# Kernel tuning notes

Measured on AMD Instinct MI355X. Metric: run time of the kernel, lower is better.

## Reference

```python
import jax, jax.numpy as jnp
import numpy as np

N = 50000        # nodes
E = 100000       # directed edges
F_NODE = 22      # atom features
F_EDGE = 4       # bond features
H = 64           # hidden_dim
EPS = 1e-5       # BatchNorm eps


def setup_inputs() -> dict:
    key = jax.random.key(0)
    ks = jax.random.split(key, 16)
    s = 0.05
    return {
        "x": jax.random.normal(ks[0], (N, F_NODE), dtype=jnp.float32),
        "edge_attr": jax.random.normal(ks[1], (E, F_EDGE), dtype=jnp.float32),
        "We1": jax.random.normal(ks[2], (F_EDGE, F_NODE * H), dtype=jnp.float32) * s,
        "be1": jnp.zeros((F_NODE * H,), dtype=jnp.float32),
        "root1": jax.random.normal(ks[3], (F_NODE, H), dtype=jnp.float32) * s,
        "b1": jnp.zeros((H,), dtype=jnp.float32),
        "g1": jnp.ones((H,), dtype=jnp.float32),
        "beta1": jnp.zeros((H,), dtype=jnp.float32),
        "We2": jax.random.normal(ks[4], (F_EDGE, H * H), dtype=jnp.float32) * s,
        "be2": jnp.zeros((H * H,), dtype=jnp.float32),
        "root2": jax.random.normal(ks[5], (H, H), dtype=jnp.float32) * s,
        "b2": jnp.zeros((H,), dtype=jnp.float32),
        "g2": jnp.ones((H,), dtype=jnp.float32),
        "beta2": jnp.zeros((H,), dtype=jnp.float32),
        "Wfc": jax.random.normal(ks[6], (H, 1), dtype=jnp.float32) * s,
        "bfc": jnp.zeros((1,), dtype=jnp.float32),
        "edge_index": jax.random.randint(ks[7], (2, E), 0, N, dtype=jnp.int32),
    }


def nnconv(x, edge_index, edge_attr, We, be, root, bias, in_ch, out_ch):
    # PyG NNConv (aggr='add', root_weight=True):
    #   out_i = x_i @ root + bias + sum_{(j->i)} x_j @ reshape(MLP(e_ji), [in, out])
    src, dst = edge_index[0], edge_index[1]
    w = jax.nn.relu(edge_attr @ We + be).reshape(-1, in_ch, out_ch)  # [E, in, out]
    msg = jnp.einsum('ei,eio->eo', x[src], w)                        # [E, out]
    agg = jax.ops.segment_sum(msg, dst, num_segments=x.shape[0])     # [N, out]
    return agg + x @ root + bias


def batchnorm(x, gamma, beta):
    # training-mode BatchNorm1d: batch statistics, biased variance
    mu = jnp.mean(x, axis=0)
    var = jnp.mean(jnp.square(x - mu), axis=0)
    return (x - mu) * jax.lax.rsqrt(var + EPS) * gamma + beta


def reference(x, edge_attr, We1, be1, root1, b1, g1, beta1,
              We2, be2, root2, b2, g2, beta2, Wfc, bfc, edge_index):
    h = nnconv(x, edge_index, edge_attr, We1, be1, root1, b1, F_NODE, H)
    h = jax.nn.relu(batchnorm(h, g1, beta1))
    # dropout is identity in eval / deterministic reference
    h = nnconv(h, edge_index, edge_attr, We2, be2, root2, b2, H, H)
    h = jax.nn.relu(batchnorm(h, g2, beta2))
    return jax.nn.sigmoid(h @ Wfc + bfc)  # [N, 1]
```

## Files before the change

### kernel.cpp

```cpp
#include <hip/hip_runtime.h>
#include <math.h>

#define N_NODES 50000
#define N_EDGES 100000
#define FNODE 22
#define HDIM 64
#define BN_EPS 1e-5f

typedef __attribute__((ext_vector_type(8))) short bfrag;
typedef __attribute__((ext_vector_type(4))) float facc;
typedef __attribute__((ext_vector_type(4))) unsigned int uint4v;

__device__ __forceinline__ float readlane_f(float v, int lane) {
    return __uint_as_float(__builtin_amdgcn_readlane(__float_as_uint(v), (unsigned)lane));
}
__device__ __forceinline__ unsigned f2bf(float x) {
    unsigned u = __float_as_uint(x);
    return (u + 0x7FFFu + ((u >> 16) & 1u)) >> 16;
}
__device__ __forceinline__ unsigned pk2bf(float lo, float hi) {
    return f2bf(lo) | (f2bf(hi) << 16);
}

__global__ void k_node1(const float* __restrict__ x, const float* __restrict__ root1,
                        const float* __restrict__ b1, float* __restrict__ h1) {
    __shared__ float rt[FNODE * HDIM];
    for (int idx = threadIdx.x; idx < FNODE * HDIM; idx += blockDim.x) rt[idx] = root1[idx];
    __syncthreads();
    int lane = threadIdx.x & 63;
    int wpb = blockDim.x >> 6;
    int wid = blockIdx.x * wpb + (threadIdx.x >> 6);
    int nw = gridDim.x * wpb;
    const int ngroups = N_NODES / 8;
    float bload = b1[lane];
    for (int g = wid; g < ngroups; g += nw) {
        int nbase = g * 8;
        float xr[8], acc[8];
#pragma unroll
        for (int e = 0; e < 8; ++e) {
            xr[e] = (lane < FNODE) ? x[(nbase + e) * FNODE + lane] : 0.f;
            acc[e] = bload;
        }
#pragma unroll
        for (int i = 0; i < FNODE; ++i) {
            float r = rt[i * HDIM + lane];
#pragma unroll
            for (int e = 0; e < 8; ++e)
                acc[e] = fmaf(readlane_f(xr[e], i), r, acc[e]);
        }
#pragma unroll
        for (int e = 0; e < 8; ++e) h1[(nbase + e) * HDIM + lane] = acc[e];
    }
}

template <int IN, int CHUNK>
__launch_bounds__(256, 4)
__global__ void k_edge(const float* __restrict__ h, const float* __restrict__ ea,
                       const float* __restrict__ We, const float* __restrict__ be,
                       const int* __restrict__ eidx, float* __restrict__ out) {
    constexpr int INH = IN * HDIM;
    __shared__ uint4v Wf[IN * 32];

    int obeg = (blockIdx.x & 1) * 32;
    int tileblk = blockIdx.x >> 1;

    for (int idx = threadIdx.x; idx < IN * 32; idx += 256) {
        int i = idx >> 5, oloc = idx & 31;
        int c = i * HDIM + obeg + oloc;
        Wf[idx] = uint4v{pk2bf(We[c], We[INH + c]),
                         pk2bf(We[2 * INH + c], We[3 * INH + c]),
                         f2bf(be[c]), 0u};
    }
    __syncthreads();

    int lane = threadIdx.x & 63;
    int e16 = lane & 15;
    int orow4 = (lane >> 4) * 4;
    int tile = tileblk * 4 + (threadIdx.x >> 6);
    int ebase = tile * 32;
    if (ebase >= N_EDGES) return;

    bool act = lane < 16;
    float4 ea0 = ((const float4*)ea)[ebase + e16];
    float4 ea1 = ((const float4*)ea)[ebase + 16 + e16];
    unsigned aone = act ? 0x3F80u : 0u;
    bfrag A0 = __builtin_bit_cast(bfrag, uint4v{act ? pk2bf(ea0.x, ea0.y) : 0u,
                                                act ? pk2bf(ea0.z, ea0.w) : 0u, aone, 0u});
    bfrag A1 = __builtin_bit_cast(bfrag, uint4v{act ? pk2bf(ea1.x, ea1.y) : 0u,
                                                act ? pk2bf(ea1.z, ea1.w) : 0u, aone, 0u});

    const float* pA[4];
    const float* pB[4];
    int dA[4], dB[4];
#pragma unroll
    for (int j = 0; j < 4; ++j) {
        pA[j] = h + (size_t)eidx[ebase + orow4 + j] * IN;
        pB[j] = h + (size_t)eidx[ebase + 16 + orow4 + j] * IN;
        dA[j] = eidx[N_EDGES + ebase + orow4 + j];
        dB[j] = eidx[N_EDGES + ebase + 16 + orow4 + j];
    }

    const facc zero4 = {0.f, 0.f, 0.f, 0.f};
    facc m0[2] = {zero4, zero4}, m1[2] = {zero4, zero4};

    for (int i0 = 0; i0 < IN; i0 += CHUNK) {
        float hA[4][CHUNK], hB[4][CHUNK];
        if constexpr (CHUNK == 4) {
#pragma unroll
            for (int j = 0; j < 4; ++j) {
                float4 v = *(const float4*)(pA[j] + i0);
                hA[j][0] = v.x; hA[j][1] = v.y; hA[j][2] = v.z; hA[j][3] = v.w;
                float4 u = *(const float4*)(pB[j] + i0);
                hB[j][0] = u.x; hB[j][1] = u.y; hB[j][2] = u.z; hB[j][3] = u.w;
            }
        } else {
#pragma unroll
            for (int j = 0; j < 4; ++j) {
                float2 v = *(const float2*)(pA[j] + i0);
                hA[j][0] = v.x; hA[j][1] = v.y;
                float2 u = *(const float2*)(pB[j] + i0);
                hB[j][0] = u.x; hB[j][1] = u.y;
            }
        }
#pragma unroll
        for (int t = 0; t < 2; ++t) {
#pragma unroll
            for (int di = 0; di < CHUNK; ++di) {
                bfrag B = __builtin_bit_cast(bfrag, Wf[(i0 + di) * 32 + t * 16 + e16]);
                facc t0 = __builtin_amdgcn_mfma_f32_16x16x32_bf16(A0, B, zero4, 0, 0, 0);
                facc t1 = __builtin_amdgcn_mfma_f32_16x16x32_bf16(A1, B, zero4, 0, 0, 0);
#pragma unroll
                for (int j = 0; j < 4; ++j) {
                    m0[t][j] = fmaf(hA[j][di], fmaxf(t0[j], 0.f), m0[t][j]);
                    m1[t][j] = fmaf(hB[j][di], fmaxf(t1[j], 0.f), m1[t][j]);
                }
            }
        }
    }

#pragma unroll
    for (int t = 0; t < 2; ++t) {
#pragma unroll
        for (int j = 0; j < 4; ++j) {
            atomicAdd(&out[(size_t)dA[j] * HDIM + obeg + t * 16 + e16], m0[t][j]);
            atomicAdd(&out[(size_t)dB[j] * HDIM + obeg + t * 16 + e16], m1[t][j]);
        }
    }
}

__global__ void k_packB(const float* __restrict__ root2, uint4v* __restrict__ Bt) {
    int t = threadIdx.x;
    int ot = t >> 6, lane = t & 63;
    int o = ot * 16 + (lane & 15);
    int kg = lane >> 4;
#pragma unroll
    for (int q = 0; q < 2; ++q) {
        int ib = q * 32 + kg * 8;
        Bt[(ot * 2 + q) * 64 + lane] =
            uint4v{pk2bf(root2[(ib + 0) * HDIM + o], root2[(ib + 1) * HDIM + o]),
                   pk2bf(root2[(ib + 2) * HDIM + o], root2[(ib + 3) * HDIM + o]),
                   pk2bf(root2[(ib + 4) * HDIM + o], root2[(ib + 5) * HDIM + o]),
                   pk2bf(root2[(ib + 6) * HDIM + o], root2[(ib + 7) * HDIM + o])};
    }
}

__global__ void k_stats(const float* __restrict__ hbuf, float* stats) {
    int c = threadIdx.x & 63;
    int r = threadIdx.x >> 6;
    int rowsPer = blockDim.x >> 6;
    float s = 0.f, q = 0.f;
    for (int n = blockIdx.x * rowsPer + r; n < N_NODES; n += gridDim.x * rowsPer) {
        float v = hbuf[n * HDIM + c];
        s += v;
        q = fmaf(v, v, q);
    }
    __shared__ float ls[4][64], lq[4][64];
    ls[r][c] = s;
    lq[r][c] = q;
    __syncthreads();
    if (r == 0) {
        s = ls[0][c] + ls[1][c] + ls[2][c] + ls[3][c];
        q = lq[0][c] + lq[1][c] + lq[2][c] + lq[3][c];
        atomicAdd(&stats[c], s);
        atomicAdd(&stats[64 + c], q);
    }
}

__global__ void k_finalize(const float* stats_in, const float* __restrict__ g,
                           const float* __restrict__ beta, float* as_out) {
    int c = threadIdx.x;
    float mu = stats_in[c] * (1.f / N_NODES);
    float var = stats_in[64 + c] * (1.f / N_NODES) - mu * mu;
    var = fmaxf(var, 0.f);
    float a = g[c] * rsqrtf(var + BN_EPS);
    as_out[c] = a;
    as_out[64 + c] = beta[c] - mu * a;
}

__global__ void k_apply1(const float* h1, const float* __restrict__ as1,
                         const uint4v* __restrict__ Bt, const float* __restrict__ b2,
                         float* __restrict__ h1n, float* h2) {
    int lane = threadIdx.x & 63;
    int m = lane & 15, kg = lane >> 4, orow4 = (lane >> 4) * 4;
    int tile = blockIdx.x * 4 + (threadIdx.x >> 6);
    int nb = tile * 16;
    if (nb >= N_NODES) return;
    int node = nb + m;
    const float* hr = h1 + (size_t)node * HDIM;

    float4 a0 = *(const float4*)(as1 + kg * 8), a1 = *(const float4*)(as1 + kg * 8 + 4);
    float4 s0 = *(const float4*)(as1 + 64 + kg * 8), s1 = *(const float4*)(as1 + 64 + kg * 8 + 4);
    float4 a2 = *(const float4*)(as1 + 32 + kg * 8), a3 = *(const float4*)(as1 + 32 + kg * 8 + 4);
    float4 s2 = *(const float4*)(as1 + 96 + kg * 8), s3 = *(const float4*)(as1 + 96 + kg * 8 + 4);

    float4 v0 = *(const float4*)(hr + kg * 8), v1 = *(const float4*)(hr + kg * 8 + 4);
    float4 v2 = *(const float4*)(hr + 32 + kg * 8), v3 = *(const float4*)(hr + 32 + kg * 8 + 4);

    float r0[8], r1[8];
#pragma unroll
    for (int p = 0; p < 4; ++p) {
        r0[p]     = fmaxf(fmaf((&v0.x)[p], (&a0.x)[p], (&s0.x)[p]), 0.f);
        r0[p + 4] = fmaxf(fmaf((&v1.x)[p], (&a1.x)[p], (&s1.x)[p]), 0.f);
        r1[p]     = fmaxf(fmaf((&v2.x)[p], (&a2.x)[p], (&s2.x)[p]), 0.f);
        r1[p + 4] = fmaxf(fmaf((&v3.x)[p], (&a3.x)[p], (&s3.x)[p]), 0.f);
    }
    *(float4*)(h1n + (size_t)node * HDIM + kg * 8)     = float4{r0[0], r0[1], r0[2], r0[3]};
    *(float4*)(h1n + (size_t)node * HDIM + kg * 8 + 4) = float4{r0[4], r0[5], r0[6], r0[7]};
    *(float4*)(h1n + (size_t)node * HDIM + 32 + kg * 8)     = float4{r1[0], r1[1], r1[2], r1[3]};
    *(float4*)(h1n + (size_t)node * HDIM + 32 + kg * 8 + 4) = float4{r1[4], r1[5], r1[6], r1[7]};

    bfrag A0 = __builtin_bit_cast(bfrag, uint4v{pk2bf(r0[0], r0[1]), pk2bf(r0[2], r0[3]),
                                                pk2bf(r0[4], r0[5]), pk2bf(r0[6], r0[7])});
    bfrag A1 = __builtin_bit_cast(bfrag, uint4v{pk2bf(r1[0], r1[1]), pk2bf(r1[2], r1[3]),
                                                pk2bf(r1[4], r1[5]), pk2bf(r1[6], r1[7])});

    const facc zero4 = {0.f, 0.f, 0.f, 0.f};
#pragma unroll
    for (int ot = 0; ot < 4; ++ot) {
        bfrag B0 = __builtin_bit_cast(bfrag, Bt[(ot * 2 + 0) * 64 + lane]);
        bfrag B1 = __builtin_bit_cast(bfrag, Bt[(ot * 2 + 1) * 64 + lane]);
        facc d = __builtin_amdgcn_mfma_f32_16x16x32_bf16(A0, B0, zero4, 0, 0, 0);
        d = __builtin_amdgcn_mfma_f32_16x16x32_bf16(A1, B1, d, 0, 0, 0);
        float bv = b2[ot * 16 + m];
#pragma unroll
        for (int j = 0; j < 4; ++j)
            h2[(size_t)(nb + orow4 + j) * HDIM + ot * 16 + m] = d[j] + bv;
    }
}

__global__ void k_final(const float* __restrict__ h2, const float* __restrict__ as2,
                        const float* __restrict__ Wfc, const float* __restrict__ bfc,
                        float* __restrict__ out) {
    int lane = threadIdx.x & 63;
    int n = blockIdx.x * (blockDim.x >> 6) + (threadIdx.x >> 6);
    if (n >= N_NODES) return;
    float a = as2[lane], s = as2[64 + lane];
    float v = fmaxf(fmaf(h2[n * HDIM + lane], a, s), 0.f) * Wfc[lane];
#pragma unroll
    for (int off = 32; off > 0; off >>= 1) v += __shfl_xor(v, off, 64);
    if (lane == 0) out[n] = 1.f / (1.f + expf(-(v + bfc[0])));
}

extern "C" void kernel_launch(void* const* d_in, const int* in_sizes, int n_in,
                              void* d_out, int out_size, void* d_ws, size_t ws_size,
                              hipStream_t stream) {
    const float* x     = (const float*)d_in[0];
    const float* ea    = (const float*)d_in[1];
    const float* We1   = (const float*)d_in[2];
    const float* be1   = (const float*)d_in[3];
    const float* root1 = (const float*)d_in[4];
    const float* b1    = (const float*)d_in[5];
    const float* g1    = (const float*)d_in[6];
    const float* beta1 = (const float*)d_in[7];
    const float* We2   = (const float*)d_in[8];
    const float* be2   = (const float*)d_in[9];
    const float* root2 = (const float*)d_in[10];
    const float* b2    = (const float*)d_in[11];
    const float* g2    = (const float*)d_in[12];
    const float* beta2 = (const float*)d_in[13];
    const float* Wfc   = (const float*)d_in[14];
    const float* bfc   = (const float*)d_in[15];
    const int*   eidx  = (const int*)d_in[16];
    float* out = (float*)d_out;

    char* ws = (char*)d_ws;
    const size_t nbuf = (size_t)N_NODES * HDIM * sizeof(float);
    float* h1    = (float*)ws;
    float* h1n   = (float*)(ws + nbuf);
    float* h2    = h1;
    float* stats = (float*)(ws + 2 * nbuf);
    uint4v* Bt   = (uint4v*)(ws + 2 * nbuf + 4096);

    hipMemsetAsync(stats, 0, 512 * sizeof(float), stream);
    k_packB<<<1, 256, 0, stream>>>(root2, Bt);

    const int edgeBlocks = 2 * ((N_EDGES / 32 + 3) / 4);
    const int nodeBlocks = (N_NODES + 3) / 4;
    const int tileBlocks = (N_NODES / 16 + 3) / 4;

    k_node1<<<512, 256, 0, stream>>>(x, root1, b1, h1);
    k_edge<FNODE, 2><<<edgeBlocks, 256, 0, stream>>>(x, ea, We1, be1, eidx, h1);
    k_stats<<<256, 256, 0, stream>>>(h1, stats);
    k_finalize<<<1, 64, 0, stream>>>(stats, g1, beta1, stats + 128);
    k_apply1<<<tileBlocks, 256, 0, stream>>>(h1, stats + 128, Bt, b2, h1n, h2);
    k_edge<HDIM, 4><<<edgeBlocks, 256, 0, stream>>>(h1n, ea, We2, be2, eidx, h2);
    k_stats<<<256, 256, 0, stream>>>(h2, stats + 256);
    k_finalize<<<1, 64, 0, stream>>>(stats + 256, g2, beta2, stats + 384);
    k_final<<<nodeBlocks, 256, 0, stream>>>(h2, stats + 384, Wfc, bfc, out);
}
```

Measured before the change: 184.8 us.

## Use MFMA for layer-1 root transform and software-prefetch gathered rows in edge kernel

Replaces the scalar readlane-based x@root1 kernel with a bf16 MFMA kernel over 16-node tiles, using a generalized k_packB template to pre-pack root1. In the edge kernel, gathered source-row chunks are double-buffered so the next chunk's loads are issued before the current chunk's MFMA/FMA work. Byte offsets are kept as 32-bit values, and destination indices are loaded only just before the atomics to lower register pressure. The cost is extra prefetch registers and bf16 rounding of x in layer 1, which was fp32 before.

```diff
diff --git a/kernel.cpp b/kernel.cpp
--- a/kernel.cpp
+++ b/kernel.cpp
@@ -11,9 +11,6 @@
 typedef __attribute__((ext_vector_type(4))) float facc;
 typedef __attribute__((ext_vector_type(4))) unsigned int uint4v;
 
-__device__ __forceinline__ float readlane_f(float v, int lane) {
-    return __uint_as_float(__builtin_amdgcn_readlane(__float_as_uint(v), (unsigned)lane));
-}
 __device__ __forceinline__ unsigned f2bf(float x) {
     unsigned u = __float_as_uint(x);
     return (u + 0x7FFFu + ((u >> 16) & 1u)) >> 16;
@@ -22,34 +19,53 @@
     return f2bf(lo) | (f2bf(hi) << 16);
 }
 
-__global__ void k_node1(const float* __restrict__ x, const float* __restrict__ root1,
+template <int K>
+__global__ void k_packB(const float* __restrict__ W, uint4v* __restrict__ Bt) {
+    constexpr int NQ = (K + 31) / 32;
+    int t = threadIdx.x;
+    int ot = t >> 6, lane = t & 63;
+    int o = ot * 16 + (lane & 15);
+    int kg = lane >> 4;
+#pragma unroll
+    for (int q = 0; q < NQ; ++q) {
+        unsigned w[4];
+#pragma unroll
+        for (int p = 0; p < 4; ++p) {
+            int k0 = q * 32 + kg * 8 + 2 * p;
+            float lo = (k0 < K) ? W[k0 * HDIM + o] : 0.f;
+            float hi = (k0 + 1 < K) ? W[(k0 + 1) * HDIM + o] : 0.f;
+            w[p] = pk2bf(lo, hi);
+        }
+        Bt[(ot * NQ + q) * 64 + lane] = uint4v{w[0], w[1], w[2], w[3]};
+    }
+}
+
+__global__ void k_node1(const float* __restrict__ x, const uint4v* __restrict__ Bt1,
                         const float* __restrict__ b1, float* __restrict__ h1) {
-    __shared__ float rt[FNODE * HDIM];
-    for (int idx = threadIdx.x; idx < FNODE * HDIM; idx += blockDim.x) rt[idx] = root1[idx];
-    __syncthreads();
     int lane = threadIdx.x & 63;
-    int wpb = blockDim.x >> 6;
-    int wid = blockIdx.x * wpb + (threadIdx.x >> 6);
-    int nw = gridDim.x * wpb;
-    const int ngroups = N_NODES / 8;
-    float bload = b1[lane];
-    for (int g = wid; g < ngroups; g += nw) {
-        int nbase = g * 8;
-        float xr[8], acc[8];
-#pragma unroll
-        for (int e = 0; e < 8; ++e) {
-            xr[e] = (lane < FNODE) ? x[(nbase + e) * FNODE + lane] : 0.f;
-            acc[e] = bload;
-        }
-#pragma unroll
-        for (int i = 0; i < FNODE; ++i) {
-            float r = rt[i * HDIM + lane];
-#pragma unroll
-            for (int e = 0; e < 8; ++e)
-                acc[e] = fmaf(readlane_f(xr[e], i), r, acc[e]);
-        }
-#pragma unroll
-        for (int e = 0; e < 8; ++e) h1[(nbase + e) * HDIM + lane] = acc[e];
+    int m = lane & 15, kg = lane >> 4, orow4 = kg * 4;
+    int tile = blockIdx.x * 4 + (threadIdx.x >> 6);
+    int nb = tile * 16;
+    if (nb >= N_NODES) return;
+    const float* xr = x + (size_t)(nb + m) * FNODE;
+    float xv[8];
+#pragma unroll
+    for (int p = 0; p < 4; ++p) {
+        int c = kg * 8 + 2 * p;
+        float2 v = (c + 1 < FNODE) ? *(const float2*)(xr + c) : float2{0.f, 0.f};
+        xv[2 * p] = v.x; xv[2 * p + 1] = v.y;
+    }
+    bfrag A = __builtin_bit_cast(bfrag, uint4v{pk2bf(xv[0], xv[1]), pk2bf(xv[2], xv[3]),
+                                               pk2bf(xv[4], xv[5]), pk2bf(xv[6], xv[7])});
+    const facc zero4 = {0.f, 0.f, 0.f, 0.f};
+#pragma unroll
+    for (int ot = 0; ot < 4; ++ot) {
+        bfrag B = __builtin_bit_cast(bfrag, Bt1[ot * 64 + lane]);
+        facc d = __builtin_amdgcn_mfma_f32_16x16x32_bf16(A, B, zero4, 0, 0, 0);
+        float bv = b1[ot * 16 + m];
+#pragma unroll
+        for (int j = 0; j < 4; ++j)
+            h1[(size_t)(nb + orow4 + j) * HDIM + ot * 16 + m] = d[j] + bv;
     }
 }
 
@@ -89,37 +105,49 @@
     bfrag A1 = __builtin_bit_cast(bfrag, uint4v{act ? pk2bf(ea1.x, ea1.y) : 0u,
                                                 act ? pk2bf(ea1.z, ea1.w) : 0u, aone, 0u});
 
-    const float* pA[4];
-    const float* pB[4];
-    int dA[4], dB[4];
+    const char* hb = (const char*)h;
+    unsigned offA[4], offB[4];
 #pragma unroll
     for (int j = 0; j < 4; ++j) {
-        pA[j] = h + (size_t)eidx[ebase + orow4 + j] * IN;
-        pB[j] = h + (size_t)eidx[ebase + 16 + orow4 + j] * IN;
-        dA[j] = eidx[N_EDGES + ebase + orow4 + j];
-        dB[j] = eidx[N_EDGES + ebase + 16 + orow4 + j];
+        offA[j] = (unsigned)eidx[ebase + orow4 + j] * (IN * 4);
+        offB[j] = (unsigned)eidx[ebase + 16 + orow4 + j] * (IN * 4);
     }
 
     const facc zero4 = {0.f, 0.f, 0.f, 0.f};
     facc m0[2] = {zero4, zero4}, m1[2] = {zero4, zero4};
 
+    float cA[4][CHUNK], cB[4][CHUNK];
+#pragma unroll
+    for (int j = 0; j < 4; ++j) {
+        if constexpr (CHUNK == 4) {
+            float4 v = *(const float4*)(hb + offA[j]);
+            cA[j][0] = v.x; cA[j][1] = v.y; cA[j][2] = v.z; cA[j][3] = v.w;
+            float4 u = *(const float4*)(hb + offB[j]);
+            cB[j][0] = u.x; cB[j][1] = u.y; cB[j][2] = u.z; cB[j][3] = u.w;
+        } else {
+            float2 v = *(const float2*)(hb + offA[j]);
+            cA[j][0] = v.x; cA[j][1] = v.y;
+            float2 u = *(const float2*)(hb + offB[j]);
+            cB[j][0] = u.x; cB[j][1] = u.y;
+        }
+    }
+
+#pragma unroll
     for (int i0 = 0; i0 < IN; i0 += CHUNK) {
-        float hA[4][CHUNK], hB[4][CHUNK];
-        if constexpr (CHUNK == 4) {
-#pragma unroll
-            for (int j = 0; j < 4; ++j) {
-                float4 v = *(const float4*)(pA[j] + i0);
-                hA[j][0] = v.x; hA[j][1] = v.y; hA[j][2] = v.z; hA[j][3] = v.w;
-                float4 u = *(const float4*)(pB[j] + i0);
-                hB[j][0] = u.x; hB[j][1] = u.y; hB[j][2] = u.z; hB[j][3] = u.w;
-            }
-        } else {
-#pragma unroll
-            for (int j = 0; j < 4; ++j) {
-                float2 v = *(const float2*)(pA[j] + i0);
-                hA[j][0] = v.x; hA[j][1] = v.y;
-                float2 u = *(const float2*)(pB[j] + i0);
-                hB[j][0] = u.x; hB[j][1] = u.y;
+        const int ip = (i0 + CHUNK < IN) ? (i0 + CHUNK) : i0;
+        float nA[4][CHUNK], nB[4][CHUNK];
+#pragma unroll
+        for (int j = 0; j < 4; ++j) {
+            if constexpr (CHUNK == 4) {
+                float4 v = *(const float4*)(hb + offA[j] + (size_t)ip * 4);
+                nA[j][0] = v.x; nA[j][1] = v.y; nA[j][2] = v.z; nA[j][3] = v.w;
+                float4 u = *(const float4*)(hb + offB[j] + (size_t)ip * 4);
+                nB[j][0] = u.x; nB[j][1] = u.y; nB[j][2] = u.z; nB[j][3] = u.w;
+            } else {
+                float2 v = *(const float2*)(hb + offA[j] + (size_t)ip * 4);
+                nA[j][0] = v.x; nA[j][1] = v.y;
+                float2 u = *(const float2*)(hb + offB[j] + (size_t)ip * 4);
+                nB[j][0] = u.x; nB[j][1] = u.y;
             }
         }
 #pragma unroll
@@ -131,13 +159,23 @@
                 facc t1 = __builtin_amdgcn_mfma_f32_16x16x32_bf16(A1, B, zero4, 0, 0, 0);
 #pragma unroll
                 for (int j = 0; j < 4; ++j) {
-                    m0[t][j] = fmaf(hA[j][di], fmaxf(t0[j], 0.f), m0[t][j]);
-                    m1[t][j] = fmaf(hB[j][di], fmaxf(t1[j], 0.f), m1[t][j]);
+                    m0[t][j] = fmaf(cA[j][di], fmaxf(t0[j], 0.f), m0[t][j]);
+                    m1[t][j] = fmaf(cB[j][di], fmaxf(t1[j], 0.f), m1[t][j]);
                 }
             }
         }
-    }
-
+#pragma unroll
+        for (int j = 0; j < 4; ++j)
+#pragma unroll
+            for (int di = 0; di < CHUNK; ++di) { cA[j][di] = nA[j][di]; cB[j][di] = nB[j][di]; }
+    }
+
+    int dA[4], dB[4];
+#pragma unroll
+    for (int j = 0; j < 4; ++j) {
+        dA[j] = eidx[N_EDGES + ebase + orow4 + j];
+        dB[j] = eidx[N_EDGES + ebase + 16 + orow4 + j];
+    }
 #pragma unroll
     for (int t = 0; t < 2; ++t) {
 #pragma unroll
@@ -145,22 +183,6 @@
             atomicAdd(&out[(size_t)dA[j] * HDIM + obeg + t * 16 + e16], m0[t][j]);
             atomicAdd(&out[(size_t)dB[j] * HDIM + obeg + t * 16 + e16], m1[t][j]);
         }
-    }
-}
-
-__global__ void k_packB(const float* __restrict__ root2, uint4v* __restrict__ Bt) {
-    int t = threadIdx.x;
-    int ot = t >> 6, lane = t & 63;
-    int o = ot * 16 + (lane & 15);
-    int kg = lane >> 4;
-#pragma unroll
-    for (int q = 0; q < 2; ++q) {
-        int ib = q * 32 + kg * 8;
-        Bt[(ot * 2 + q) * 64 + lane] =
-            uint4v{pk2bf(root2[(ib + 0) * HDIM + o], root2[(ib + 1) * HDIM + o]),
-                   pk2bf(root2[(ib + 2) * HDIM + o], root2[(ib + 3) * HDIM + o]),
-                   pk2bf(root2[(ib + 4) * HDIM + o], root2[(ib + 5) * HDIM + o]),
-                   pk2bf(root2[(ib + 6) * HDIM + o], root2[(ib + 7) * HDIM + o])};
     }
 }
 
@@ -289,20 +311,22 @@
     float* h1n   = (float*)(ws + nbuf);
     float* h2    = h1;
     float* stats = (float*)(ws + 2 * nbuf);
-    uint4v* Bt   = (uint4v*)(ws + 2 * nbuf + 4096);
+    uint4v* Bt2  = (uint4v*)(ws + 2 * nbuf + 4096);
+    uint4v* Bt1  = (uint4v*)(ws + 2 * nbuf + 4096 + 8192);
 
     hipMemsetAsync(stats, 0, 512 * sizeof(float), stream);
-    k_packB<<<1, 256, 0, stream>>>(root2, Bt);
+    k_packB<HDIM><<<1, 256, 0, stream>>>(root2, Bt2);
+    k_packB<FNODE><<<1, 256, 0, stream>>>(root1, Bt1);
 
     const int edgeBlocks = 2 * ((N_EDGES / 32 + 3) / 4);
     const int nodeBlocks = (N_NODES + 3) / 4;
     const int tileBlocks = (N_NODES / 16 + 3) / 4;
 
-    k_node1<<<512, 256, 0, stream>>>(x, root1, b1, h1);
+    k_node1<<<tileBlocks, 256, 0, stream>>>(x, Bt1, b1, h1);
     k_edge<FNODE, 2><<<edgeBlocks, 256, 0, stream>>>(x, ea, We1, be1, eidx, h1);
     k_stats<<<256, 256, 0, stream>>>(h1, stats);
     k_finalize<<<1, 64, 0, stream>>>(stats, g1, beta1, stats + 128);
-    k_apply1<<<tileBlocks, 256, 0, stream>>>(h1, stats + 128, Bt, b2, h1n, h2);
+    k_apply1<<<tileBlocks, 256, 0, stream>>>(h1, stats + 128, Bt2, b2, h1n, h2);
     k_edge<HDIM, 4><<<edgeBlocks, 256, 0, stream>>>(h1n, ea, We2, be2, eidx, h2);
     k_stats<<<256, 256, 0, stream>>>(h2, stats + 256);
     k_finalize<<<1, 64, 0, stream>>>(stats + 256, g2, beta2, stats + 384);
```

Result: no change. 184.6 us (-0.1%).
